# Kernel optimization log

Measured on AMD Instinct MI355X. Metric: run time of the kernel, lower is better.

## Reference

```python
import jax, jax.numpy as jnp
import numpy as np

B, S, D = 16, 2048, 256
SCALE = 1.0 / np.sqrt(D).astype(np.float32)

def setup_inputs() -> dict:
    key = jax.random.key(0)
    k1, k2, k3, k4 = jax.random.split(key, 4)
    x = jax.random.normal(k1, (B, S, D), dtype=jnp.float32)
    w_qkv = jax.random.normal(k2, (3 * D, D), dtype=jnp.float32) * (1.0 / np.sqrt(D))
    w_out = jax.random.normal(k3, (D, D), dtype=jnp.float32) * (1.0 / np.sqrt(D))
    b_out = jax.random.normal(k4, (D,), dtype=jnp.float32) * 0.01
    return {"x": x, "w_qkv": w_qkv, "w_out": w_out, "b_out": b_out}

def reference(x, w_qkv, w_out, b_out):
    # qkv: [B, S, 3D] = x @ W_qkv^T (torch Linear convention)
    qkv = jnp.einsum('bsd,ed->bse', x, w_qkv)
    q, k, v = jnp.split(qkv, 3, axis=-1)  # each [B, S, D]
    scores = jnp.einsum('bsd,btd->bst', q, k) * SCALE  # [B, S, S]
    attn = jax.nn.softmax(scores, axis=-1)  # dropout = identity (eval mode)
    ctx = jnp.einsum('bst,btd->bsd', attn, v)  # [B, S, D]
    out = jnp.einsum('bsd,ed->bse', ctx, w_out) + b_out
    return out
```

## Files before the change

kernel.cpp:

```cpp
#include <hip/hip_runtime.h>
#include <hip/hip_bf16.h>


typedef short bf16x8 __attribute__((ext_vector_type(8)));
typedef float f32x4 __attribute__((ext_vector_type(4)));

#define MFMA16(a, b, c) __builtin_amdgcn_mfma_f32_16x16x32_bf16((a), (b), (c), 0, 0, 0)

__device__ __forceinline__ unsigned short f2bf(float f) {
  unsigned int x;
  __builtin_memcpy(&x, &f, 4);
  x = x + 0x7fffu + ((x >> 16) & 1u);
  return (unsigned short)(x >> 16);
}
__device__ __forceinline__ unsigned int pack2(float a, float b) {
  float2 t;
  t.x = a;
  t.y = b;
  __hip_bfloat162 h = __float22bfloat162_rn(t);
  unsigned int u;
  __builtin_memcpy(&u, &h, 4);
  return u;
}

typedef __attribute__((address_space(3))) void as3_void;
typedef __attribute__((address_space(1))) const void as1_void;
__device__ __forceinline__ void gl_lds16(const void* g, void* l) {
  __builtin_amdgcn_global_load_lds((as1_void*)(unsigned long long)g,
                                   (as3_void*)(unsigned int)(unsigned long long)l,
                                   16, 0, 0);
}

__global__ __launch_bounds__(256, 4) void cvtw_kernel(
    const float* __restrict__ W, unsigned short* __restrict__ Wbf) {
  int idx = blockIdx.x * 256 + threadIdx.x;
  int row = idx >> 5, sc = idx & 31;
  int c = (sc & 24) | ((sc ^ (row & 7)) & 7);
  const float* wp = W + (size_t)row * 256 + c * 8;
  float4 a0 = *(const float4*)wp, a1 = *(const float4*)(wp + 4);
  uint4 u;
  u.x = pack2(a0.x, a0.y);
  u.y = pack2(a0.z, a0.w);
  u.z = pack2(a1.x, a1.y);
  u.w = pack2(a1.z, a1.w);
  *(uint4*)(Wbf + (size_t)idx * 8) = u;
}

__global__ __launch_bounds__(512, 1) void qkv_kernel(
    const float* __restrict__ X, const unsigned short* __restrict__ Wqbf,
    unsigned short* __restrict__ Q, unsigned short* __restrict__ Kp,
    unsigned short* __restrict__ Vt) {
  __shared__ unsigned short Al[128 * 256];
  __shared__ unsigned short Bl[128 * 256];
  const int m0 = blockIdx.x * 128;
  const int t = threadIdx.x;
  const int w = t >> 6, lane = t & 63, lo = lane & 15, quad = lane >> 4;
  const int wr = (w >> 2) * 64, wc = (w & 3) * 32;

#pragma unroll
  for (int r = 0; r < 8; ++r) {
    int ci = r * 512 + t;
    int row = ci >> 5, c = ci & 31;
    int s = (c & 24) | ((c ^ (row & 7)) & 7);
    const float* xp = X + (size_t)(m0 + row) * 256 + c * 8;
    float4 a0 = *(const float4*)xp, a1 = *(const float4*)(xp + 4);
    uint4 ua;
    ua.x = pack2(a0.x, a0.y);
    ua.y = pack2(a0.z, a0.w);
    ua.z = pack2(a1.x, a1.y);
    ua.w = pack2(a1.z, a1.w);
    *(uint4*)(&Al[row * 256 + s * 8]) = ua;
  }

  for (int n = 0; n < 6; ++n) {
    const int n0 = n * 128;
    if (n > 0) __syncthreads();
    {
      const unsigned short* Wb = Wqbf + (size_t)n0 * 256;
      int lofs = __builtin_amdgcn_readfirstlane(w * 64 * 8);
#pragma unroll
      for (int r = 0; r < 8; ++r) {
        gl_lds16(Wb + (size_t)(r * 512 + t) * 8, &Bl[r * 512 * 8 + lofs]);
      }
    }
    asm volatile("s_waitcnt vmcnt(0)" ::: "memory");
    __syncthreads();

    f32x4 zero4 = {0.f, 0.f, 0.f, 0.f};
    f32x4 acc[4][2];
#pragma unroll
    for (int i = 0; i < 4; i++)
#pragma unroll
      for (int j = 0; j < 2; j++) acc[i][j] = zero4;

#pragma unroll
    for (int kc = 0; kc < 8; ++kc) {
      const int c = kc * 4 + quad;
      const int jj = (c & 24) | ((c ^ (lo & 7)) & 7);
      bf16x8 af[4], bfr[2];
#pragma unroll
      for (int mt = 0; mt < 4; ++mt)
        af[mt] = *(const bf16x8*)(&Al[(wr + mt * 16 + lo) * 256 + jj * 8]);
#pragma unroll
      for (int nt = 0; nt < 2; ++nt)
        bfr[nt] = *(const bf16x8*)(&Bl[(wc + nt * 16 + lo) * 256 + jj * 8]);
#pragma unroll
      for (int mt = 0; mt < 4; ++mt)
#pragma unroll
        for (int nt = 0; nt < 2; ++nt)
          acc[mt][nt] = MFMA16(af[mt], bfr[nt], acc[mt][nt]);
    }

    const int mb = m0 + wr, nb = n0 + wc;
    if (n0 < 256) {
#pragma unroll
      for (int mt = 0; mt < 4; ++mt)
#pragma unroll
        for (int nt = 0; nt < 2; ++nt) {
          int m = mb + mt * 16 + quad * 4;
          int nn = nb + nt * 16 + lo;
          unsigned short* p = Q + (size_t)m * 256 + nn;
          p[0] = f2bf(acc[mt][nt][0]);
          p[256] = f2bf(acc[mt][nt][1]);
          p[512] = f2bf(acc[mt][nt][2]);
          p[768] = f2bf(acc[mt][nt][3]);
        }
    } else if (n0 < 512) {
#pragma unroll
      for (int mt = 0; mt < 4; ++mt)
#pragma unroll
        for (int nt = 0; nt < 2; ++nt) {
          int m = mb + mt * 16 + quad * 4;
          int nn = nb + nt * 16 + lo - 256;
          unsigned short* p = Kp + (size_t)m * 256 + nn;
          p[0] = f2bf(acc[mt][nt][0]);
          p[256] = f2bf(acc[mt][nt][1]);
          p[512] = f2bf(acc[mt][nt][2]);
          p[768] = f2bf(acc[mt][nt][3]);
        }
    } else {
#pragma unroll
      for (int mt = 0; mt < 4; ++mt)
#pragma unroll
        for (int nt = 0; nt < 2; ++nt) {
          int m = mb + mt * 16 + quad * 4;
          int d = nb + nt * 16 + lo - 512;
          int b = m >> 11, s = m & 2047;
          uint2 v;
          v.x = pack2(acc[mt][nt][0], acc[mt][nt][1]);
          v.y = pack2(acc[mt][nt][2], acc[mt][nt][3]);
          *(uint2*)(Vt + ((size_t)(b * 256 + d)) * 2048 + s) = v;
        }
    }
  }
}

__global__ __launch_bounds__(512, 2) void attn_kernel(
    const unsigned short* __restrict__ Q, const unsigned short* __restrict__ K,
    const unsigned short* __restrict__ Vt, unsigned short* __restrict__ C) {
  __shared__ __attribute__((aligned(16))) unsigned short smem[65536];
  const int id = blockIdx.x;
  const int b = id & 15;
  const int qt = id >> 4;
  const int t = threadIdx.x;
  const int w = t >> 6, lane = t & 63, lo = lane & 15, quad = lane >> 4;
  constexpr float SCALE_LOG2E = 0.0625f * 1.4426950408889634f;

  const unsigned short* Kb = K + (size_t)b * 2048 * 256;
  const unsigned short* Vb = Vt + (size_t)b * 256 * 2048;

  unsigned int gkoff[4], gvoff[4];
  int loK[4], loV[4];
#pragma unroll
  for (int r = 0; r < 4; ++r) {
    int ck = r * 512 + t;
    int row = ck >> 5, j = ck & 31;
    int srcj = (j & 16) | ((j ^ (row & 15)) & 15);
    gkoff[r] = (unsigned int)((row * 256 + srcj * 8) * 2);
    loK[r] = __builtin_amdgcn_readfirstlane((r * 512 + w * 64) * 8);

    int cv = r * 512 + t;
    int d = cv >> 3, slot = cv & 7;
    int g = slot ^ (d & 7);
    gvoff[r] = (unsigned int)((d * 2048 + g * 8) * 2);
    loV[r] = __builtin_amdgcn_readfirstlane(16384 + (r * 512 + w * 64) * 8);
  }

  const int qrow = b * 2048 + qt * 128 + w * 16 + lo;
  const unsigned short* qp = Q + (size_t)qrow * 256;
  bf16x8 qf[8];
#pragma unroll
  for (int ks = 0; ks < 8; ++ks)
    qf[ks] = *(const bf16x8*)(qp + ks * 32 + quad * 8);

  f32x4 zero4 = {0.f, 0.f, 0.f, 0.f};
  f32x4 oacc[16];
#pragma unroll
  for (int i = 0; i < 16; i++) oacc[i] = zero4;
  float m_run = -1e30f, l_run = 0.f;

#pragma unroll
  for (int r = 0; r < 4; ++r) {
    gl_lds16((const char*)Kb + gkoff[r], &smem[loK[r]]);
    gkoff[r] += 64 * 256 * 2;
  }
#pragma unroll
  for (int r = 0; r < 4; ++r) {
    gl_lds16((const char*)Vb + gvoff[r], &smem[loV[r]]);
    gvoff[r] += 64 * 2;
  }

  for (int it = 0; it < 32; ++it) {
    asm volatile("s_waitcnt vmcnt(0)" ::: "memory");
    __syncthreads();
    if (it < 31) {
      const int pn = ((it + 1) & 1) * 32768;
#pragma unroll
      for (int r = 0; r < 4; ++r) {
        gl_lds16((const char*)Kb + gkoff[r], &smem[pn + loK[r]]);
        gkoff[r] += 64 * 256 * 2;
      }
#pragma unroll
      for (int r = 0; r < 4; ++r) {
        gl_lds16((const char*)Vb + gvoff[r], &smem[pn + loV[r]]);
        gvoff[r] += 64 * 2;
      }
    }
    const unsigned short* Kl = smem + (it & 1) * 32768;
    const unsigned short* Vl = Kl + 16384;

    f32x4 sacc[4];
#pragma unroll
    for (int r = 0; r < 4; ++r) sacc[r] = zero4;
    __builtin_amdgcn_s_setprio(1);
#pragma unroll
    for (int ks = 0; ks < 8; ++ks) {
      const int c = ks * 4 + quad;
      const int jj = (c & 16) | ((c ^ lo) & 15);
#pragma unroll
      for (int r = 0; r < 4; ++r) {
        bf16x8 kf = *(const bf16x8*)(&Kl[(r * 16 + lo) * 256 + jj * 8]);
        sacc[r] = MFMA16(kf, qf[ks], sacc[r]);
      }
    }
    __builtin_amdgcn_s_setprio(0);

    float p[4][4];
    float cmax = -1e30f;
#pragma unroll
    for (int r = 0; r < 4; r++)
#pragma unroll
      for (int i = 0; i < 4; i++) {
        p[r][i] = sacc[r][i] * SCALE_LOG2E;
        cmax = fmaxf(cmax, p[r][i]);
      }
    cmax = fmaxf(cmax, __shfl_xor(cmax, 16));
    cmax = fmaxf(cmax, __shfl_xor(cmax, 32));
    if (!__all(cmax <= m_run + 8.f)) {
      float mnew = fmaxf(m_run, cmax);
      float alpha = exp2f(m_run - mnew);
      l_run *= alpha;
#pragma unroll
      for (int i = 0; i < 16; i++) oacc[i] *= alpha;
      m_run = mnew;
    }
    float rsum = 0.f;
#pragma unroll
    for (int r = 0; r < 4; r++)
#pragma unroll
      for (int i = 0; i < 4; i++) {
        p[r][i] = exp2f(p[r][i] - m_run);
        rsum += p[r][i];
      }
    rsum += __shfl_xor(rsum, 16);
    rsum += __shfl_xor(rsum, 32);
    l_run += rsum;

    unsigned int pk[4][2];
#pragma unroll
    for (int r = 0; r < 4; r++) {
      pk[r][0] = pack2(p[r][0], p[r][1]);
      pk[r][1] = pack2(p[r][2], p[r][3]);
    }

#pragma unroll
    for (int ks2 = 0; ks2 < 2; ++ks2) {
      union {
        unsigned int u[4];
        bf16x8 v;
      } cvt;
#pragma unroll
      for (int dd = 0; dd < 4; ++dd) {
        int src = lo + 16 * ((2 * quad + (dd >> 1)) & 3);
        unsigned int v0 = (unsigned int)__shfl((int)pk[2 * ks2][dd & 1], src);
        unsigned int v1 = (unsigned int)__shfl((int)pk[2 * ks2 + 1][dd & 1], src);
        cvt.u[dd] = (quad >> 1) ? v1 : v0;
      }
      bf16x8 pf = cvt.v;
      __builtin_amdgcn_s_setprio(1);
#pragma unroll
      for (int dt = 0; dt < 16; ++dt) {
        int slot = (ks2 * 4 + quad) ^ (lo & 7);
        bf16x8 vf = *(const bf16x8*)(&Vl[(dt * 16 + lo) * 64 + slot * 8]);
        oacc[dt] = MFMA16(vf, pf, oacc[dt]);
      }
      __builtin_amdgcn_s_setprio(0);
    }
  }

  float inv = 1.0f / l_run;
  unsigned short* cp = C + (size_t)qrow * 256;
#pragma unroll
  for (int dt = 0; dt < 16; ++dt) {
    uint2 v;
    v.x = pack2(oacc[dt][0] * inv, oacc[dt][1] * inv);
    v.y = pack2(oacc[dt][2] * inv, oacc[dt][3] * inv);
    *(uint2*)(cp + dt * 16 + quad * 4) = v;
  }
}

__global__ __launch_bounds__(512, 1) void proj_kernel(
    const unsigned short* __restrict__ Xc, const float* __restrict__ W,
    const float* __restrict__ bias, float* __restrict__ out) {
  __shared__ unsigned short Al[128 * 256];
  __shared__ unsigned short Bl[128 * 256];
  const int m0 = blockIdx.x * 128;
  const int t = threadIdx.x;
  const int w = t >> 6, lane = t & 63, lo = lane & 15, quad = lane >> 4;
  const int wr = (w >> 2) * 64, wc = (w & 3) * 32;

  const unsigned short* Xb = Xc + (size_t)m0 * 256;
#pragma unroll
  for (int r = 0; r < 8; ++r) {
    int idx = r * 512 + t;
    int row = idx >> 5, sc = idx & 31;
    int c = (sc & 24) | ((sc ^ (row & 7)) & 7);
    int lofs = __builtin_amdgcn_readfirstlane((r * 512 + w * 64) * 8);
    gl_lds16(Xb + (size_t)row * 256 + c * 8, &Al[lofs]);
  }

  for (int n = 0; n < 2; ++n) {
    const int n0 = n * 128;
    if (n > 0) __syncthreads();
#pragma unroll
    for (int r = 0; r < 8; ++r) {
      int ci = r * 512 + t;
      int row = ci >> 5, c = ci & 31;
      int s = (c & 24) | ((c ^ (row & 7)) & 7);
      const float* wp = W + (size_t)(n0 + row) * 256 + c * 8;
      float4 b0 = *(const float4*)wp, b1 = *(const float4*)(wp + 4);
      uint4 ub;
      ub.x = pack2(b0.x, b0.y);
      ub.y = pack2(b0.z, b0.w);
      ub.z = pack2(b1.x, b1.y);
      ub.w = pack2(b1.z, b1.w);
      *(uint4*)(&Bl[row * 256 + s * 8]) = ub;
    }
    if (n == 0) asm volatile("s_waitcnt vmcnt(0)" ::: "memory");
    __syncthreads();

    f32x4 zero4 = {0.f, 0.f, 0.f, 0.f};
    f32x4 acc[4][2];
#pragma unroll
    for (int i = 0; i < 4; i++)
#pragma unroll
      for (int j = 0; j < 2; j++) acc[i][j] = zero4;

#pragma unroll
    for (int kc = 0; kc < 8; ++kc) {
      const int c = kc * 4 + quad;
      const int jj = (c & 24) | ((c ^ (lo & 7)) & 7);
      bf16x8 af[4], bfr[2];
#pragma unroll
      for (int mt = 0; mt < 4; ++mt)
        af[mt] = *(const bf16x8*)(&Al[(wr + mt * 16 + lo) * 256 + jj * 8]);
#pragma unroll
      for (int nt = 0; nt < 2; ++nt)
        bfr[nt] = *(const bf16x8*)(&Bl[(wc + nt * 16 + lo) * 256 + jj * 8]);
#pragma unroll
      for (int mt = 0; mt < 4; ++mt)
#pragma unroll
        for (int nt = 0; nt < 2; ++nt)
          acc[mt][nt] = MFMA16(af[mt], bfr[nt], acc[mt][nt]);
    }

    const int mb = m0 + wr, nb = n0 + wc;
#pragma unroll
    for (int nt = 0; nt < 2; ++nt) {
      int nn = nb + nt * 16 + lo;
      float bv = bias[nn];
#pragma unroll
      for (int mt = 0; mt < 4; ++mt) {
        int m = mb + mt * 16 + quad * 4;
        float* p = out + (size_t)m * 256 + nn;
        p[0] = acc[mt][nt][0] + bv;
        p[256] = acc[mt][nt][1] + bv;
        p[512] = acc[mt][nt][2] + bv;
        p[768] = acc[mt][nt][3] + bv;
      }
    }
  }
}

extern "C" void kernel_launch(void* const* d_in, const int* in_sizes, int n_in,
                              void* d_out, int out_size, void* d_ws, size_t ws_size,
                              hipStream_t stream) {
  const float* X = (const float*)d_in[0];
  const float* Wq = (const float*)d_in[1];
  const float* Wo = (const float*)d_in[2];
  const float* Bo = (const float*)d_in[3];
  float* out = (float*)d_out;
  unsigned short* ws = (unsigned short*)d_ws;

  const size_t NE = (size_t)16 * 2048 * 256;
  unsigned short* Qb = ws;
  unsigned short* Kb = ws + NE;
  unsigned short* Vt = ws + 2 * NE;
  unsigned short* Cx = ws;
  unsigned short* Wqbf = (unsigned short*)d_out;

  cvtw_kernel<<<dim3(96), 256, 0, stream>>>(Wq, Wqbf);
  qkv_kernel<<<dim3(256), 512, 0, stream>>>(X, Wqbf, Qb, Kb, Vt);
  attn_kernel<<<dim3(256), 512, 0, stream>>>(Qb, Kb, Vt, Cx);
  proj_kernel<<<dim3(256), 512, 0, stream>>>(Cx, Wo, Bo, out);
}
```

Before: 212.2 us.

## Fuse output projection into attention epilogue and shrink QKV tiles

The attention kernel now keeps the normalized context in registers, loads W_out into shared memory as bf16, and performs the output projection plus bias directly. This removes the separate projection kernel and the round trip of the context through global memory. Separately, the QKV GEMM switches to 64-row tiles with 256-thread blocks and 512 blocks to improve occupancy and load balance. The fused epilogue adds per-block W_out conversion work (256 blocks each converting the full 256x256 matrix) and extra register pressure in the attention kernel.

```diff
diff --git a/kernel.cpp b/kernel.cpp
--- a/kernel.cpp
+++ b/kernel.cpp
@@ -46,20 +46,20 @@
   *(uint4*)(Wbf + (size_t)idx * 8) = u;
 }
 
-__global__ __launch_bounds__(512, 1) void qkv_kernel(
+__global__ __launch_bounds__(256, 2) void qkv_kernel(
     const float* __restrict__ X, const unsigned short* __restrict__ Wqbf,
     unsigned short* __restrict__ Q, unsigned short* __restrict__ Kp,
     unsigned short* __restrict__ Vt) {
-  __shared__ unsigned short Al[128 * 256];
-  __shared__ unsigned short Bl[128 * 256];
-  const int m0 = blockIdx.x * 128;
+  __shared__ unsigned short Al[64 * 256];
+  __shared__ unsigned short Bl[64 * 256];
+  const int m0 = blockIdx.x * 64;
   const int t = threadIdx.x;
   const int w = t >> 6, lane = t & 63, lo = lane & 15, quad = lane >> 4;
-  const int wr = (w >> 2) * 64, wc = (w & 3) * 32;
+  const int wr = (w >> 1) * 32, wc = (w & 1) * 32;
 
 #pragma unroll
   for (int r = 0; r < 8; ++r) {
-    int ci = r * 512 + t;
+    int ci = r * 256 + t;
     int row = ci >> 5, c = ci & 31;
     int s = (c & 24) | ((c ^ (row & 7)) & 7);
     const float* xp = X + (size_t)(m0 + row) * 256 + c * 8;
@@ -72,24 +72,23 @@
     *(uint4*)(&Al[row * 256 + s * 8]) = ua;
   }
 
-  for (int n = 0; n < 6; ++n) {
-    const int n0 = n * 128;
+  const int lofs = __builtin_amdgcn_readfirstlane(w * 64 * 8);
+  for (int n = 0; n < 12; ++n) {
+    const int n0 = n * 64;
     if (n > 0) __syncthreads();
     {
       const unsigned short* Wb = Wqbf + (size_t)n0 * 256;
-      int lofs = __builtin_amdgcn_readfirstlane(w * 64 * 8);
-#pragma unroll
-      for (int r = 0; r < 8; ++r) {
-        gl_lds16(Wb + (size_t)(r * 512 + t) * 8, &Bl[r * 512 * 8 + lofs]);
-      }
+#pragma unroll
+      for (int r = 0; r < 8; ++r)
+        gl_lds16(Wb + (size_t)(r * 256 + t) * 8, &Bl[r * 256 * 8 + lofs]);
     }
     asm volatile("s_waitcnt vmcnt(0)" ::: "memory");
     __syncthreads();
 
     f32x4 zero4 = {0.f, 0.f, 0.f, 0.f};
-    f32x4 acc[4][2];
-#pragma unroll
-    for (int i = 0; i < 4; i++)
+    f32x4 acc[2][2];
+#pragma unroll
+    for (int i = 0; i < 2; i++)
 #pragma unroll
       for (int j = 0; j < 2; j++) acc[i][j] = zero4;
 
@@ -97,15 +96,15 @@
     for (int kc = 0; kc < 8; ++kc) {
       const int c = kc * 4 + quad;
       const int jj = (c & 24) | ((c ^ (lo & 7)) & 7);
-      bf16x8 af[4], bfr[2];
-#pragma unroll
-      for (int mt = 0; mt < 4; ++mt)
+      bf16x8 af[2], bfr[2];
+#pragma unroll
+      for (int mt = 0; mt < 2; ++mt)
         af[mt] = *(const bf16x8*)(&Al[(wr + mt * 16 + lo) * 256 + jj * 8]);
 #pragma unroll
       for (int nt = 0; nt < 2; ++nt)
         bfr[nt] = *(const bf16x8*)(&Bl[(wc + nt * 16 + lo) * 256 + jj * 8]);
 #pragma unroll
-      for (int mt = 0; mt < 4; ++mt)
+      for (int mt = 0; mt < 2; ++mt)
 #pragma unroll
         for (int nt = 0; nt < 2; ++nt)
           acc[mt][nt] = MFMA16(af[mt], bfr[nt], acc[mt][nt]);
@@ -114,7 +113,7 @@
     const int mb = m0 + wr, nb = n0 + wc;
     if (n0 < 256) {
 #pragma unroll
-      for (int mt = 0; mt < 4; ++mt)
+      for (int mt = 0; mt < 2; ++mt)
 #pragma unroll
         for (int nt = 0; nt < 2; ++nt) {
           int m = mb + mt * 16 + quad * 4;
@@ -127,7 +126,7 @@
         }
     } else if (n0 < 512) {
 #pragma unroll
-      for (int mt = 0; mt < 4; ++mt)
+      for (int mt = 0; mt < 2; ++mt)
 #pragma unroll
         for (int nt = 0; nt < 2; ++nt) {
           int m = mb + mt * 16 + quad * 4;
@@ -140,7 +139,7 @@
         }
     } else {
 #pragma unroll
-      for (int mt = 0; mt < 4; ++mt)
+      for (int mt = 0; mt < 2; ++mt)
 #pragma unroll
         for (int nt = 0; nt < 2; ++nt) {
           int m = mb + mt * 16 + quad * 4;
@@ -157,7 +156,8 @@
 
 __global__ __launch_bounds__(512, 2) void attn_kernel(
     const unsigned short* __restrict__ Q, const unsigned short* __restrict__ K,
-    const unsigned short* __restrict__ Vt, unsigned short* __restrict__ C) {
+    const unsigned short* __restrict__ Vt, const float* __restrict__ Wo,
+    const float* __restrict__ bias, float* __restrict__ out) {
   __shared__ __attribute__((aligned(16))) unsigned short smem[65536];
   const int id = blockIdx.x;
   const int b = id & 15;
@@ -309,96 +309,77 @@
   }
 
   float inv = 1.0f / l_run;
-  unsigned short* cp = C + (size_t)qrow * 256;
+  uint2 c2[16];
 #pragma unroll
   for (int dt = 0; dt < 16; ++dt) {
-    uint2 v;
-    v.x = pack2(oacc[dt][0] * inv, oacc[dt][1] * inv);
-    v.y = pack2(oacc[dt][2] * inv, oacc[dt][3] * inv);
-    *(uint2*)(cp + dt * 16 + quad * 4) = v;
-  }
-}
-
-__global__ __launch_bounds__(512, 1) void proj_kernel(
-    const unsigned short* __restrict__ Xc, const float* __restrict__ W,
-    const float* __restrict__ bias, float* __restrict__ out) {
-  __shared__ unsigned short Al[128 * 256];
-  __shared__ unsigned short Bl[128 * 256];
-  const int m0 = blockIdx.x * 128;
-  const int t = threadIdx.x;
-  const int w = t >> 6, lane = t & 63, lo = lane & 15, quad = lane >> 4;
-  const int wr = (w >> 2) * 64, wc = (w & 3) * 32;
-
-  const unsigned short* Xb = Xc + (size_t)m0 * 256;
-#pragma unroll
-  for (int r = 0; r < 8; ++r) {
-    int idx = r * 512 + t;
-    int row = idx >> 5, sc = idx & 31;
-    int c = (sc & 24) | ((sc ^ (row & 7)) & 7);
-    int lofs = __builtin_amdgcn_readfirstlane((r * 512 + w * 64) * 8);
-    gl_lds16(Xb + (size_t)row * 256 + c * 8, &Al[lofs]);
-  }
-
-  for (int n = 0; n < 2; ++n) {
-    const int n0 = n * 128;
-    if (n > 0) __syncthreads();
-#pragma unroll
-    for (int r = 0; r < 8; ++r) {
-      int ci = r * 512 + t;
-      int row = ci >> 5, c = ci & 31;
-      int s = (c & 24) | ((c ^ (row & 7)) & 7);
-      const float* wp = W + (size_t)(n0 + row) * 256 + c * 8;
-      float4 b0 = *(const float4*)wp, b1 = *(const float4*)(wp + 4);
-      uint4 ub;
-      ub.x = pack2(b0.x, b0.y);
-      ub.y = pack2(b0.z, b0.w);
-      ub.z = pack2(b1.x, b1.y);
-      ub.w = pack2(b1.z, b1.w);
-      *(uint4*)(&Bl[row * 256 + s * 8]) = ub;
-    }
-    if (n == 0) asm volatile("s_waitcnt vmcnt(0)" ::: "memory");
-    __syncthreads();
-
-    f32x4 zero4 = {0.f, 0.f, 0.f, 0.f};
-    f32x4 acc[4][2];
-#pragma unroll
-    for (int i = 0; i < 4; i++)
-#pragma unroll
-      for (int j = 0; j < 2; j++) acc[i][j] = zero4;
-
-#pragma unroll
-    for (int kc = 0; kc < 8; ++kc) {
-      const int c = kc * 4 + quad;
-      const int jj = (c & 24) | ((c ^ (lo & 7)) & 7);
-      bf16x8 af[4], bfr[2];
-#pragma unroll
-      for (int mt = 0; mt < 4; ++mt)
-        af[mt] = *(const bf16x8*)(&Al[(wr + mt * 16 + lo) * 256 + jj * 8]);
-#pragma unroll
-      for (int nt = 0; nt < 2; ++nt)
-        bfr[nt] = *(const bf16x8*)(&Bl[(wc + nt * 16 + lo) * 256 + jj * 8]);
-#pragma unroll
-      for (int mt = 0; mt < 4; ++mt)
-#pragma unroll
-        for (int nt = 0; nt < 2; ++nt)
-          acc[mt][nt] = MFMA16(af[mt], bfr[nt], acc[mt][nt]);
-    }
-
-    const int mb = m0 + wr, nb = n0 + wc;
-#pragma unroll
-    for (int nt = 0; nt < 2; ++nt) {
-      int nn = nb + nt * 16 + lo;
-      float bv = bias[nn];
-#pragma unroll
-      for (int mt = 0; mt < 4; ++mt) {
-        int m = mb + mt * 16 + quad * 4;
-        float* p = out + (size_t)m * 256 + nn;
-        p[0] = acc[mt][nt][0] + bv;
-        p[256] = acc[mt][nt][1] + bv;
-        p[512] = acc[mt][nt][2] + bv;
-        p[768] = acc[mt][nt][3] + bv;
-      }
-    }
+    c2[dt].x = pack2(oacc[dt][0] * inv, oacc[dt][1] * inv);
+    c2[dt].y = pack2(oacc[dt][2] * inv, oacc[dt][3] * inv);
+  }
+
+  __syncthreads();
+#pragma unroll
+  for (int r = 0; r < 16; ++r) {
+    int ci = r * 512 + t;
+    int row = ci >> 5, c = ci & 31;
+    int s = (c & 24) | ((c ^ (row & 7)) & 7);
+    const float* wp = Wo + (size_t)row * 256 + c * 8;
+    float4 a0 = *(const float4*)wp, a1 = *(const float4*)(wp + 4);
+    uint4 ua;
+    ua.x = pack2(a0.x, a0.y);
+    ua.y = pack2(a0.z, a0.w);
+    ua.z = pack2(a1.x, a1.y);
+    ua.w = pack2(a1.z, a1.w);
+    *(uint4*)(&smem[row * 256 + s * 8]) = ua;
+  }
+  __syncthreads();
+
+  f32x4 outacc[16];
+#pragma unroll
+  for (int i = 0; i < 16; i++) outacc[i] = zero4;
+
+#pragma unroll
+  for (int ks = 0; ks < 8; ++ks) {
+    int sa = lo + 16 * ((quad & 1) * 2);
+    unsigned int xA = (unsigned int)__shfl((int)c2[2 * ks].x, sa);
+    unsigned int yA = (unsigned int)__shfl((int)c2[2 * ks].y, sa);
+    unsigned int xB = (unsigned int)__shfl((int)c2[2 * ks].x, sa + 16);
+    unsigned int yB = (unsigned int)__shfl((int)c2[2 * ks].y, sa + 16);
+    unsigned int xA1 = (unsigned int)__shfl((int)c2[2 * ks + 1].x, sa);
+    unsigned int yA1 = (unsigned int)__shfl((int)c2[2 * ks + 1].y, sa);
+    unsigned int xB1 = (unsigned int)__shfl((int)c2[2 * ks + 1].x, sa + 16);
+    unsigned int yB1 = (unsigned int)__shfl((int)c2[2 * ks + 1].y, sa + 16);
+    union {
+      unsigned int u[4];
+      bf16x8 v;
+    } cvt;
+    bool hiq = (quad >> 1) != 0;
+    cvt.u[0] = hiq ? xA1 : xA;
+    cvt.u[1] = hiq ? yA1 : yA;
+    cvt.u[2] = hiq ? xB1 : xB;
+    cvt.u[3] = hiq ? yB1 : yB;
+    bf16x8 pf = cvt.v;
+
+    const int c = ks * 4 + quad;
+    const int jj = (c & 24) | ((c ^ (lo & 7)) & 7);
+    __builtin_amdgcn_s_setprio(1);
+#pragma unroll
+    for (int et = 0; et < 16; ++et) {
+      bf16x8 af = *(const bf16x8*)(&smem[(et * 16 + lo) * 256 + jj * 8]);
+      outacc[et] = MFMA16(af, pf, outacc[et]);
+    }
+    __builtin_amdgcn_s_setprio(0);
+  }
+
+  float* op = out + (size_t)qrow * 256;
+#pragma unroll
+  for (int et = 0; et < 16; ++et) {
+    const float4 b4 = *(const float4*)(bias + et * 16 + quad * 4);
+    float4 v;
+    v.x = outacc[et][0] + b4.x;
+    v.y = outacc[et][1] + b4.y;
+    v.z = outacc[et][2] + b4.z;
+    v.w = outacc[et][3] + b4.w;
+    *(float4*)(op + et * 16 + quad * 4) = v;
   }
 }
 
@@ -416,11 +397,9 @@
   unsigned short* Qb = ws;
   unsigned short* Kb = ws + NE;
   unsigned short* Vt = ws + 2 * NE;
-  unsigned short* Cx = ws;
   unsigned short* Wqbf = (unsigned short*)d_out;
 
   cvtw_kernel<<<dim3(96), 256, 0, stream>>>(Wq, Wqbf);
-  qkv_kernel<<<dim3(256), 512, 0, stream>>>(X, Wqbf, Qb, Kb, Vt);
-  attn_kernel<<<dim3(256), 512, 0, stream>>>(Qb, Kb, Vt, Cx);
-  proj_kernel<<<dim3(256), 512, 0, stream>>>(Cx, Wo, Bo, out);
-}
+  qkv_kernel<<<dim3(512), 256, 0, stream>>>(X, Wqbf, Qb, Kb, Vt);
+  attn_kernel<<<dim3(256), 512, 0, stream>>>(Qb, Kb, Vt, Wo, Bo, out);
+}
```

New measurement: 204.8 us. 1.04x faster.
